# Performance work log

Hardware: AMD Instinct MI355X
Metric: run time of the kernel (lower is better)

## Reference

```python
import jax, jax.numpy as jnp
import numpy as np

D_MODEL, N, L_MAX, BATCH = 512, 64, 2048, 8


def _make_s4_buffers(n):
    # HiPPO-NPLR: hippo[i,j] = sqrt(2i+1)sqrt(2j+1) if i>j; i+1 if i==j (1-indexed)
    i = np.arange(1, n + 1)
    row = np.sqrt(2 * i + 1.0)
    hippo = np.tril(np.outer(row, row), -1) + np.diag(i + 1.0)
    p = 0.5 * np.sqrt(2 * i + 1.0)
    q = 2.0 * p
    S = -hippo + np.outer(p, q)
    lam, V = np.linalg.eig(S)
    Vc = V.conj().T
    return Vc @ p, Vc @ q, lam  # complex128 -> cast to complex64 later


def setup_inputs() -> dict:
    key = jax.random.key(0)
    k1, k2, k3, k4 = jax.random.split(key, 4)
    xavier_std = float(np.sqrt(2.0 / (N + D_MODEL)))
    p, q, lam = _make_s4_buffers(N)
    u = jax.random.normal(k1, (BATCH, L_MAX, D_MODEL), jnp.float32)
    B = jax.random.normal(k2, (D_MODEL, N), jnp.float32) * xavier_std
    Ct = jax.random.normal(k3, (D_MODEL, N), jnp.float32) * xavier_std
    D = jnp.ones((D_MODEL,), jnp.float32)
    log_step = (jax.random.uniform(k4, (D_MODEL,), jnp.float32)
                * (np.log(0.1) - np.log(0.001)) + np.log(0.001))
    return {
        "u": u, "B": B, "Ct": Ct, "D": D, "log_step": log_step,
        "p": jnp.asarray(p, jnp.complex64),
        "q": jnp.asarray(q, jnp.complex64),
        "lam": jnp.asarray(lam, jnp.complex64),
    }


def _s4_forward(u, B, Ct, D, log_step, p, q, lam):
    L = u.shape[1]  # l_max
    omega = jnp.exp((2j * np.pi / L) * jnp.arange(L)).astype(jnp.complex64)  # (L,)
    step = jnp.exp(log_step)                                                 # (d,)
    g = (2.0 / step)[:, None] * ((1.0 - omega) / (1.0 + omega))[None, :]     # (d, L)
    c = 2.0 / (1.0 + omega)                                                  # (L,)
    Bc = B.astype(jnp.complex64)
    Ctc = Ct.astype(jnp.complex64)  # Ct is real -> conj is identity
    v00 = Ctc * Bc                              # (d, n)
    v01 = Ctc * p[None, :]                      # (d, n)
    v10 = jnp.conj(q)[None, :] * Bc             # (d, n)
    v11 = jnp.broadcast_to(jnp.conj(q) * p, v00.shape)
    V = jnp.stack([v00, v01, v10, v11], 0)      # (4, d, n)
    # fused Cauchy reduction: k[k,d,l] = sum_n V[k,d,n] / (g[d,l] - lam[n])
    recip = 1.0 / (g[:, :, None] - lam[None, None, :])  # (d, L, n) big intermediate
    k00, k01, k10, k11 = jnp.einsum('kdn,dln->kdl', V, recip)
    at_roots = c * (k00 - k01 * k10 / (1.0 + k11))      # (d, L)
    # ifft + index reversal (i -> (L - i) mod L), keep real part
    order = (L - jnp.arange(L)) % L
    K = jnp.fft.ifft(at_roots, n=L, axis=-1)[:, order].real.astype(jnp.float32)  # (d, L)
    # non-circular convolution via length-2L FFT
    ud = jnp.fft.rfft(jnp.pad(u, ((0, 0), (0, L), (0, 0))), axis=1)   # (B, L+1, d)
    Kd = jnp.fft.rfft(jnp.pad(K, ((0, 0), (0, L))), axis=-1)          # (d, L+1)
    y = jnp.fft.irfft(jnp.swapaxes(ud, 1, 2) * Kd[None], axis=-1)[..., :L]  # (B, d, L)
    return jnp.swapaxes(y, 1, 2) + D[None, None, :] * u


def reference(u, B, Ct, D, log_step, p, q, lam):
    return _s4_forward(u, B, Ct, D, log_step, p, q, lam)
```

## Files before the change

### kernel.cpp

```cpp
#include <hip/hip_runtime.h>
#include <math.h>

#define D_MODEL 512
#define NSTATE  64
#define LSEQ    2048
#define L2X     4096
#define NBATCH  8
#define NT      512

#define SQ2H 0.70710678118654752f
#define C16  0.92387953251128674f
#define S16  0.38268343236508977f
#define A4096 (-1.5339807878856412e-3f)

__device__ __forceinline__ float2 cmulf(float2 a, float2 b) {
    return make_float2(a.x * b.x - a.y * b.y, a.x * b.y + a.y * b.x);
}
__device__ __forceinline__ float2 cmulc(float2 a, float2 w) {
    return make_float2(a.x * w.x + a.y * w.y, a.y * w.x - a.x * w.y);
}
__device__ __forceinline__ float2 cadd(float2 a, float2 b) { return make_float2(a.x + b.x, a.y + b.y); }
__device__ __forceinline__ float2 csub(float2 a, float2 b) { return make_float2(a.x - b.x, a.y - b.y); }
__device__ __forceinline__ float rcpf(float x) { return __builtin_amdgcn_rcpf(x); }
__device__ __forceinline__ float2 cdiv_fast(float2 a, float2 b) {
    float inv = rcpf(b.x * b.x + b.y * b.y);
    return make_float2((a.x * b.x + a.y * b.y) * inv, (a.y * b.x - a.x * b.y) * inv);
}
__device__ __forceinline__ int finitef(float v) {
    return (v == v) && (v < 3.0e38f) && (v > -3.0e38f);
}
__device__ __forceinline__ int hexrev12(int x) {
    return ((x & 15) << 8) | (x & 240) | ((x >> 8) & 15);
}

__device__ __forceinline__ int tidx(int i) { return i + (i >> 4); }
__device__ __forceinline__ int kswz(int i) { return i ^ (i >> 6); }

#define TW_SZ  1088
#define BUF_SZ 4352

__device__ __forceinline__ float2 twget4(const float2* tw, int k) {
    float2 w = tw[tidx(k & 1023)];
    if (k & 1024) w = make_float2(w.y, -w.x);
    if (k & 2048) w = make_float2(-w.x, -w.y);
    return w;
}
__device__ __forceinline__ void build_tw(float2* tw) {
    for (int k = threadIdx.x; k < 1024; k += NT) {
        float s, c;
        sincosf(A4096 * (float)k, &s, &c);
        tw[tidx(k)] = make_float2(c, s);
    }
}

__device__ __forceinline__ float2 ldc(const float* f, int n, int mode) {
    if (mode == 0) return make_float2(f[n], 0.0f);
    if (mode == 1) return make_float2(f[n], f[64 + n]);
    return make_float2(f[2 * n], f[2 * n + 1]);
}

__device__ __forceinline__ void dft4f(float2 a, float2 b, float2 c, float2 d, float2* F) {
    float2 t0 = cadd(a, c), t1 = csub(a, c);
    float2 t2 = cadd(b, d), t3 = csub(b, d);
    F[0] = cadd(t0, t2);
    F[1] = make_float2(t1.x + t3.y, t1.y - t3.x);
    F[2] = csub(t0, t2);
    F[3] = make_float2(t1.x - t3.y, t1.y + t3.x);
}
__device__ __forceinline__ void dft4i(float2 a, float2 b, float2 c, float2 d, float2* F) {
    float2 t0 = cadd(a, c), t1 = csub(a, c);
    float2 t2 = cadd(b, d), t3 = csub(b, d);
    F[0] = cadd(t0, t2);
    F[1] = make_float2(t1.x - t3.y, t1.y + t3.x);
    F[2] = csub(t0, t2);
    F[3] = make_float2(t1.x + t3.y, t1.y - t3.x);
}
__device__ __forceinline__ void dft8f(const float2* a, float2* X) {
    float2 E[4], O[4];
    dft4f(a[0], a[2], a[4], a[6], E);
    dft4f(a[1], a[3], a[5], a[7], O);
    float2 o1 = make_float2(SQ2H * (O[1].x + O[1].y), SQ2H * (O[1].y - O[1].x));
    float2 o2 = make_float2(O[2].y, -O[2].x);
    float2 o3 = make_float2(SQ2H * (O[3].y - O[3].x), -SQ2H * (O[3].x + O[3].y));
    X[0] = cadd(E[0], O[0]); X[4] = csub(E[0], O[0]);
    X[1] = cadd(E[1], o1);   X[5] = csub(E[1], o1);
    X[2] = cadd(E[2], o2);   X[6] = csub(E[2], o2);
    X[3] = cadd(E[3], o3);   X[7] = csub(E[3], o3);
}
__device__ __forceinline__ void dft8i(const float2* a, float2* X) {
    float2 E[4], O[4];
    dft4i(a[0], a[2], a[4], a[6], E);
    dft4i(a[1], a[3], a[5], a[7], O);
    float2 o1 = make_float2(SQ2H * (O[1].x - O[1].y), SQ2H * (O[1].y + O[1].x));
    float2 o2 = make_float2(-O[2].y, O[2].x);
    float2 o3 = make_float2(-SQ2H * (O[3].x + O[3].y), SQ2H * (O[3].x - O[3].y));
    X[0] = cadd(E[0], O[0]); X[4] = csub(E[0], O[0]);
    X[1] = cadd(E[1], o1);   X[5] = csub(E[1], o1);
    X[2] = cadd(E[2], o2);   X[6] = csub(E[2], o2);
    X[3] = cadd(E[3], o3);   X[7] = csub(E[3], o3);
}
__device__ __forceinline__ void dft16f(const float2* a, float2* X) {
    float2 ev[8], od[8], E[8], O[8];
    #pragma unroll
    for (int r = 0; r < 8; r++) { ev[r] = a[2 * r]; od[r] = a[2 * r + 1]; }
    dft8f(ev, E); dft8f(od, O);
    float2 t0 = O[0];
    float2 t1 = cmulf(O[1], make_float2(C16, -S16));
    float2 t2 = make_float2(SQ2H * (O[2].x + O[2].y), SQ2H * (O[2].y - O[2].x));
    float2 t3 = cmulf(O[3], make_float2(S16, -C16));
    float2 t4 = make_float2(O[4].y, -O[4].x);
    float2 t5 = cmulf(O[5], make_float2(-S16, -C16));
    float2 t6 = make_float2(SQ2H * (O[6].y - O[6].x), -SQ2H * (O[6].x + O[6].y));
    float2 t7 = cmulf(O[7], make_float2(-C16, -S16));
    X[0] = cadd(E[0], t0); X[8]  = csub(E[0], t0);
    X[1] = cadd(E[1], t1); X[9]  = csub(E[1], t1);
    X[2] = cadd(E[2], t2); X[10] = csub(E[2], t2);
    X[3] = cadd(E[3], t3); X[11] = csub(E[3], t3);
    X[4] = cadd(E[4], t4); X[12] = csub(E[4], t4);
    X[5] = cadd(E[5], t5); X[13] = csub(E[5], t5);
    X[6] = cadd(E[6], t6); X[14] = csub(E[6], t6);
    X[7] = cadd(E[7], t7); X[15] = csub(E[7], t7);
}
__device__ __forceinline__ void dft16i(const float2* a, float2* X) {
    float2 ev[8], od[8], E[8], O[8];
    #pragma unroll
    for (int r = 0; r < 8; r++) { ev[r] = a[2 * r]; od[r] = a[2 * r + 1]; }
    dft8i(ev, E); dft8i(od, O);
    float2 t0 = O[0];
    float2 t1 = cmulf(O[1], make_float2(C16, S16));
    float2 t2 = make_float2(SQ2H * (O[2].x - O[2].y), SQ2H * (O[2].x + O[2].y));
    float2 t3 = cmulf(O[3], make_float2(S16, C16));
    float2 t4 = make_float2(-O[4].y, O[4].x);
    float2 t5 = cmulf(O[5], make_float2(-S16, C16));
    float2 t6 = make_float2(-SQ2H * (O[6].x + O[6].y), SQ2H * (O[6].x - O[6].y));
    float2 t7 = cmulf(O[7], make_float2(-C16, S16));
    X[0] = cadd(E[0], t0); X[8]  = csub(E[0], t0);
    X[1] = cadd(E[1], t1); X[9]  = csub(E[1], t1);
    X[2] = cadd(E[2], t2); X[10] = csub(E[2], t2);
    X[3] = cadd(E[3], t3); X[11] = csub(E[3], t3);
    X[4] = cadd(E[4], t4); X[12] = csub(E[4], t4);
    X[5] = cadd(E[5], t5); X[13] = csub(E[5], t5);
    X[6] = cadd(E[6], t6); X[14] = csub(E[6], t6);
    X[7] = cadd(E[7], t7); X[15] = csub(E[7], t7);
}

template<int H, bool TW>
__device__ __forceinline__ void r16_dif_ld(float2* buf, const float2* twp, int t) {
    const int j = t & (H - 1);
    const int i0 = ((t - j) << 4) + j;
    const int base = i0 + (i0 >> 4);
    constexpr int S = (H >= 16) ? (H + (H >> 4)) : 1;
    float2 a[16], X[16];
    #pragma unroll
    for (int k = 0; k < 16; k++) a[k] = buf[base + k * S];
    dft16f(a, X);
    buf[base] = X[0];
    #pragma unroll
    for (int m = 1; m < 16; m++) {
        float2 v = X[m];
        if (TW) v = cmulf(v, twp[(m - 1) * 16 + j]);
        buf[base + m * S] = v;
    }
}
template<int H, bool TW>
__device__ __forceinline__ void r16_dit_ld(float2* buf, const float2* twp, int t) {
    const int j = t & (H - 1);
    const int i0 = ((t - j) << 4) + j;
    const int base = i0 + (i0 >> 4);
    constexpr int S = (H >= 16) ? (H + (H >> 4)) : 1;
    float2 a[16], X[16];
    a[0] = buf[base];
    #pragma unroll
    for (int k = 1; k < 16; k++) {
        float2 v = buf[base + k * S];
        if (TW) v = cmulc(v, twp[(k - 1) * 16 + j]);
        a[k] = v;
    }
    dft16i(a, X);
    #pragma unroll
    for (int m = 0; m < 16; m++) buf[base + m * S] = X[m];
}

template<int H, int F, int TWMODE, int NBF>
__device__ __forceinline__ void r8_dif_stage(float2* buf, const float2* tw, const float2* twp) {
    __syncthreads();
    const int tid = threadIdx.x;
    if (NBF >= NT || tid < NBF) {
        const int j = tid & (H - 1);
        const int i0 = ((tid - j) << 3) + j;
        float2 a[8], X[8];
        #pragma unroll
        for (int k = 0; k < 8; k++) a[k] = buf[tidx(i0 + k * H)];
        dft8f(a, X);
        if (TWMODE == 1) {
            #pragma unroll
            for (int m = 1; m < 8; m++) X[m] = cmulf(X[m], twp[(m - 1) * H + j]);
        } else if (TWMODE == 2) {
            #pragma unroll
            for (int m = 1; m < 8; m++) X[m] = cmulf(X[m], twget4(tw, (j * F * m) & 4095));
        }
        #pragma unroll
        for (int m = 0; m < 8; m++) buf[tidx(i0 + m * H)] = X[m];
    }
}
__device__ __forceinline__ void r4_dif_h1(float2* buf) {
    __syncthreads();
    const int tid = threadIdx.x;
    const int i0 = tid << 2;
    float2 F[4];
    dft4f(buf[tidx(i0)], buf[tidx(i0 + 1)], buf[tidx(i0 + 2)], buf[tidx(i0 + 3)], F);
    #pragma unroll
    for (int m = 0; m < 4; m++) buf[tidx(i0 + m)] = F[m];
}

__global__ __launch_bounds__(NT) void s4_khat_kernel(
    const float* __restrict__ Bmat, const float* __restrict__ Ct,
    const float* __restrict__ log_step,
    const float* __restrict__ pf, const float* __restrict__ qf,
    const float* __restrict__ lf,
    float2* __restrict__ Khat, int size_hint)
{
    __shared__ float2 tw[TW_SZ];
    __shared__ float2 buf[BUF_SZ];
    __shared__ float2 stash[289];
    __shared__ float2 twK2[224];
    __shared__ float2 twK3[28];
    __shared__ float2 twp2[240];
    const int d = blockIdx.x;
    const int tid = threadIdx.x;

    build_tw(tw);
    if (tid < 224) { int m = (tid >> 5) + 1, j = tid & 31; float s, c;
        sincosf(A4096 * (float)(16 * j * m), &s, &c); twK2[tid] = make_float2(c, s); }
    else if (tid < 252) { int r = tid - 224; int m = (r >> 3) + 1, j = r & 7; float s, c;
        sincosf(A4096 * (float)(128 * j * m), &s, &c); twK3[r] = make_float2(c, s); }
    else if (tid < 492) { int r = tid - 252; int m = (r >> 4) + 1, j = r & 15; float s, c;
        sincosf(A4096 * (float)(16 * j * m), &s, &c); twp2[r] = make_float2(c, s); }

    int mode;
    if (size_hint >= 128) {
        mode = (fabsf(lf[1] + 0.5f) < 0.05f) ? 1 : 2;
    } else {
        float s1 = 0.0f, s2 = 0.0f;
        bool ok = true;
        for (int n = 0; n < 64; n++) {
            float v = lf[64 + n];
            if (!finitef(v)) { ok = false; break; }
            s1 += v; s2 += fabsf(v);
        }
        mode = (ok && s2 > 0.5f && s2 < 1.0e6f && fabsf(s1) < 1.0e-2f * s2) ? 1 : 0;
    }

    float2* v01  = stash;
    float2* v10  = stash + 64;
    float2* v11  = stash + 128;
    float2* lamS = stash + 192;
    float*  v00  = (float*)(stash + 256);

    if (tid < NSTATE) {
        int n = tid;
        float Bdn = Bmat[d * NSTATE + n];
        float Cdn = Ct[d * NSTATE + n];
        float2 pn = ldc(pf, n, mode);
        float2 qn = ldc(qf, n, mode);
        float2 qc = make_float2(qn.x, -qn.y);
        v00[n]  = Cdn * Bdn;
        v01[n]  = make_float2(Cdn * pn.x, Cdn * pn.y);
        v10[n]  = make_float2(qc.x * Bdn, qc.y * Bdn);
        v11[n]  = cmulf(qc, pn);
        lamS[n] = ldc(lf, n, mode);
    }
    const float two_over_step = 2.0f / expf(log_step[d]);
    __syncthreads();

    float gyr[2], tanl[2];
    float2 a00[2], a01[2], a10[2], a11[2];
    #pragma unroll
    for (int i = 0; i < 2; i++) {
        int l = tid + i * NT;
        float2 w = twget4(tw, 2 * l);
        float cth = w.x, sth = -w.y;
        float tl = sth * rcpf(1.0f + cth);
        tanl[i] = tl;
        gyr[i]  = -two_over_step * tl;
        a00[i] = make_float2(0.f, 0.f); a01[i] = make_float2(0.f, 0.f);
        a10[i] = make_float2(0.f, 0.f); a11[i] = make_float2(0.f, 0.f);
    }
    for (int n = 0; n < NSTATE; n++) {
        float2 ln = lamS[n];
        float  c0 = v00[n];
        float2 c1 = v01[n], c2 = v10[n], c3 = v11[n];
        float dxn = -ln.x;
        float dx2 = ln.x * ln.x;
        #pragma unroll
        for (int i = 0; i < 2; i++) {
            float dy = gyr[i] - ln.y;
            float ir = rcpf(fmaf(dy, dy, dx2));
            float rx = dxn * ir, ry = -dy * ir;
            a00[i].x += c0 * rx;               a00[i].y += c0 * ry;
            a01[i].x += c1.x * rx - c1.y * ry; a01[i].y += c1.x * ry + c1.y * rx;
            a10[i].x += c2.x * rx - c2.y * ry; a10[i].y += c2.x * ry + c2.y * rx;
            a11[i].x += c3.x * rx - c3.y * ry; a11[i].y += c3.x * ry + c3.y * rx;
        }
    }
    __syncthreads();
    #pragma unroll
    for (int i = 0; i < 2; i++) {
        int l = tid + i * NT;
        float2 cl = make_float2(1.0f, -tanl[i]);
        float2 onep = make_float2(1.0f + a11[i].x, a11[i].y);
        float2 corr = cdiv_fast(cmulf(a01[i], a10[i]), onep);
        float2 ar = cmulf(cl, csub(a00[i], corr));
        if (!finitef(ar.x) || !finitef(ar.y)) ar = make_float2(0.0f, 0.0f);
        buf[tidx(l)] = ar;
        if (l > 0) buf[tidx(2048 - l)] = make_float2(ar.x, -ar.y);
    }
    if (tid == 0) buf[tidx(1024)] = make_float2(0.0f, 0.0f);

    r8_dif_stage<256, 2, 2, 256>(buf, tw, nullptr);
    r8_dif_stage<32, 0, 1, 256>(buf, tw, twK2);
    r8_dif_stage<4, 0, 1, 256>(buf, tw, twK3);
    r4_dif_h1(buf);
    __syncthreads();

    const float inv2048 = 1.0f / 2048.0f;
    float krv[4]; int tpos[4];
    #pragma unroll
    for (int i = 0; i < 4; i++) {
        int p = tid + i * NT;
        tpos[i] = (p >> 8) | (((p >> 5) & 7) << 3) | (((p >> 2) & 7) << 6) | ((p & 3) << 9);
        krv[i] = buf[tidx(p)].x * inv2048;
    }
    __syncthreads();
    float* kfp = (float*)buf;
    #pragma unroll
    for (int i = 0; i < 4; i++) kfp[kswz(tpos[i])] = krv[i];
    __syncthreads();

    float a8[8];
    if (tid < 256) {
        #pragma unroll
        for (int k = 0; k < 8; k++) a8[k] = kfp[kswz(tid + 256 * k)];
    }
    __syncthreads();
    if (tid < 256) {
        const int j = tid;
        float2 ar8[8], bq[8], E[8], O[8], X[16];
        #pragma unroll
        for (int k = 0; k < 8; k++) ar8[k] = make_float2(a8[k], 0.0f);
        dft8f(ar8, E);
        bq[0] = make_float2(a8[0], 0.0f);
        bq[1] = make_float2(C16 * a8[1], -S16 * a8[1]);
        bq[2] = make_float2(SQ2H * a8[2], -SQ2H * a8[2]);
        bq[3] = make_float2(S16 * a8[3], -C16 * a8[3]);
        bq[4] = make_float2(0.0f, -a8[4]);
        bq[5] = make_float2(-S16 * a8[5], -C16 * a8[5]);
        bq[6] = make_float2(-SQ2H * a8[6], -SQ2H * a8[6]);
        bq[7] = make_float2(-C16 * a8[7], -S16 * a8[7]);
        dft8f(bq, O);
        #pragma unroll
        for (int r = 0; r < 8; r++) { X[2 * r] = E[r]; X[2 * r + 1] = O[r]; }
        const int base = j + (j >> 4);
        buf[base] = X[0];
        #pragma unroll
        for (int m = 1; m < 16; m++)
            buf[base + 272 * m] = cmulf(X[m], twget4(tw, j * m));
    }
    __syncthreads();
    if (tid < 256) r16_dif_ld<16, true>(buf, twp2, tid);
    __syncthreads();
    if (tid < 256) r16_dif_ld<1, false>(buf, nullptr, tid);
    __syncthreads();

    const float inv4096 = 1.0f / 4096.0f;
    for (int k = tid; k < L2X; k += NT) {
        float2 v = buf[tidx(k)];
        float vx = v.x * inv4096, vy = v.y * inv4096;
        if (!finitef(vx)) vx = 0.0f;
        if (!finitef(vy)) vy = 0.0f;
        Khat[(size_t)d * L2X + k] = make_float2(vx, vy);
    }
}

__global__ __launch_bounds__(NT) void conv_kernel(
    const float* __restrict__ u, const float2* __restrict__ Khat,
    const float* __restrict__ Dvec, float* __restrict__ out)
{
    __shared__ float2 tw[TW_SZ];
    __shared__ float2 bufs[2 * BUF_SZ];
    __shared__ float2 twp2[240];
    const int blk = blockIdx.x;
    const int d0 = blk >> 2;
    const int bp = blk & 3;
    const int tid = threadIdx.x;
    const int half = tid >> 8;
    const int jj = tid & 255;
    const int b = bp * 2 + half;
    float2* buf = bufs + half * BUF_SZ;

    build_tw(tw);
    if (tid < 240) { int m = (tid >> 4) + 1, j = tid & 15; float s, c;
        sincosf(A4096 * (float)(16 * j * m), &s, &c); twp2[tid] = make_float2(c, s); }

    const float* ub = u + (size_t)b * LSEQ * D_MODEL + 2 * d0;
    float2 ureg[8];
    #pragma unroll
    for (int k = 0; k < 8; k++)
        ureg[k] = *(const float2*)(ub + (size_t)(jj + 256 * k) * D_MODEL);

    __syncthreads();

    {
        float2 E[8], O[8], bq[8], X[16];
        dft8f(ureg, E);
        bq[0] = ureg[0];
        bq[1] = cmulf(ureg[1], make_float2(C16, -S16));
        bq[2] = make_float2(SQ2H * (ureg[2].x + ureg[2].y), SQ2H * (ureg[2].y - ureg[2].x));
        bq[3] = cmulf(ureg[3], make_float2(S16, -C16));
        bq[4] = make_float2(ureg[4].y, -ureg[4].x);
        bq[5] = cmulf(ureg[5], make_float2(-S16, -C16));
        bq[6] = make_float2(SQ2H * (ureg[6].y - ureg[6].x), -SQ2H * (ureg[6].x + ureg[6].y));
        bq[7] = cmulf(ureg[7], make_float2(-C16, -S16));
        dft8f(bq, O);
        #pragma unroll
        for (int r = 0; r < 8; r++) { X[2 * r] = E[r]; X[2 * r + 1] = O[r]; }
        const int base = jj + (jj >> 4);
        buf[base] = X[0];
        #pragma unroll
        for (int m = 1; m < 16; m++)
            buf[base + 272 * m] = cmulf(X[m], twget4(tw, jj * m));
    }
    __syncthreads();
    r16_dif_ld<16, true>(buf, twp2, jj);
    __syncthreads();
    r16_dif_ld<1, false>(buf, nullptr, jj);
    __syncthreads();

    const float2* K0 = Khat + (size_t)(2 * d0) * L2X;
    const float2* K1 = K0 + L2X;
    for (int t0 = jj; t0 < L2X; t0 += 256) {
        int fr = hexrev12(t0);
        int jm = hexrev12((L2X - fr) & (L2X - 1));
        if (t0 > jm) continue;
        float2 Zk = buf[tidx(t0)], Zm = buf[tidx(jm)];
        float2 U0 = make_float2(0.5f * (Zk.x + Zm.x), 0.5f * (Zk.y - Zm.y));
        float2 U1 = make_float2(0.5f * (Zk.y + Zm.y), 0.5f * (Zm.x - Zk.x));
        float2 Y0 = cmulf(U0, K0[t0]);
        float2 Y1 = cmulf(U1, K1[t0]);
        buf[tidx(t0)] = make_float2(Y0.x - Y1.y, Y0.y + Y1.x);
        buf[tidx(jm)] = make_float2(Y0.x + Y1.y, Y1.x - Y0.y);
    }
    __syncthreads();
    r16_dit_ld<1, false>(buf, nullptr, jj);
    __syncthreads();
    r16_dit_ld<16, true>(buf, twp2, jj);
    __syncthreads();

    const float dv0 = Dvec[2 * d0];
    const float dv1 = Dvec[2 * d0 + 1];
    {
        const int base = jj + (jj >> 4);
        float2 a[16];
        a[0] = buf[base];
        #pragma unroll
        for (int k = 1; k < 16; k++)
            a[k] = cmulc(buf[base + 272 * k], twget4(tw, jj * k));
        float2 ev[8], od[8], E[8], O[8];
        #pragma unroll
        for (int r = 0; r < 8; r++) { ev[r] = a[2 * r]; od[r] = a[2 * r + 1]; }
        dft8i(ev, E); dft8i(od, O);
        float2 t[8];
        t[0] = O[0];
        t[1] = cmulf(O[1], make_float2(C16, S16));
        t[2] = make_float2(SQ2H * (O[2].x - O[2].y), SQ2H * (O[2].x + O[2].y));
        t[3] = cmulf(O[3], make_float2(S16, C16));
        t[4] = make_float2(-O[4].y, O[4].x);
        t[5] = cmulf(O[5], make_float2(-S16, C16));
        t[6] = make_float2(-SQ2H * (O[6].x + O[6].y), SQ2H * (O[6].x - O[6].y));
        t[7] = cmulf(O[7], make_float2(-C16, S16));
        #pragma unroll
        for (int m = 0; m < 8; m++) {
            float2 y = cadd(E[m], t[m]);
            float o0 = y.x + dv0 * ureg[m].x;
            float o1 = y.y + dv1 * ureg[m].y;
            if (!finitef(o0)) o0 = 4.0e5f;
            if (!finitef(o1)) o1 = 4.0e5f;
            *(float2*)(out + ((size_t)b * LSEQ + jj + 256 * m) * D_MODEL + 2 * d0) = make_float2(o0, o1);
        }
    }
}

extern "C" void kernel_launch(void* const* d_in, const int* in_sizes, int n_in,
                              void* d_out, int out_size, void* d_ws, size_t ws_size,
                              hipStream_t stream) {
    (void)n_in; (void)out_size; (void)ws_size;
    const float* u        = (const float*)d_in[0];
    const float* Bmat     = (const float*)d_in[1];
    const float* Ct       = (const float*)d_in[2];
    const float* Dvec     = (const float*)d_in[3];
    const float* log_step = (const float*)d_in[4];
    const float* pf       = (const float*)d_in[5];
    const float* qf       = (const float*)d_in[6];
    const float* lf       = (const float*)d_in[7];
    float* out = (float*)d_out;

    int size_hint = in_sizes[5];

    float2* Khat = (float2*)d_ws;

    s4_khat_kernel<<<D_MODEL, NT, 0, stream>>>(Bmat, Ct, log_step, pf, qf, lf, Khat, size_hint);
    conv_kernel<<<NBATCH * (D_MODEL / 4), NT, 0, stream>>>(u, Khat, Dvec, out);
}
```

Baseline: 184.5 us.

## Shrink conv blocks to one batch and replace twiddle table with recurrence

The convolution kernel now runs 256-thread blocks that each handle one batch element and one channel pair, instead of 512-thread blocks covering two batches. The shared-memory twiddle table built per block is dropped, and the outer-stage twiddles are computed by repeated complex multiplication of a per-thread base twiddle from one sincosf. This cuts shared memory and table setup per block and allows more resident blocks. In exchange the recurrence adds a serial chain of complex multiplies, slight precision drift, and more blocks each reading Khat.

```diff
diff --git a/kernel.cpp b/kernel.cpp
--- a/kernel.cpp
+++ b/kernel.cpp
@@ -7,6 +7,7 @@
 #define L2X     4096
 #define NBATCH  8
 #define NT      512
+#define CNT     256
 
 #define SQ2H 0.70710678118654752f
 #define C16  0.92387953251128674f
@@ -382,25 +383,23 @@
     }
 }
 
-__global__ __launch_bounds__(NT) void conv_kernel(
+__global__ __launch_bounds__(CNT) void conv_kernel(
     const float* __restrict__ u, const float2* __restrict__ Khat,
     const float* __restrict__ Dvec, float* __restrict__ out)
 {
-    __shared__ float2 tw[TW_SZ];
-    __shared__ float2 bufs[2 * BUF_SZ];
+    __shared__ float2 buf[BUF_SZ];
     __shared__ float2 twp2[240];
     const int blk = blockIdx.x;
-    const int d0 = blk >> 2;
-    const int bp = blk & 3;
-    const int tid = threadIdx.x;
-    const int half = tid >> 8;
-    const int jj = tid & 255;
-    const int b = bp * 2 + half;
-    float2* buf = bufs + half * BUF_SZ;
-
-    build_tw(tw);
-    if (tid < 240) { int m = (tid >> 4) + 1, j = tid & 15; float s, c;
-        sincosf(A4096 * (float)(16 * j * m), &s, &c); twp2[tid] = make_float2(c, s); }
+    const int d0 = blk >> 3;
+    const int b  = blk & 7;
+    const int jj = threadIdx.x;
+
+    if (jj < 240) { int m = (jj >> 4) + 1, j = jj & 15; float s, c;
+        sincosf(A4096 * (float)(16 * j * m), &s, &c); twp2[jj] = make_float2(c, s); }
+
+    float sj, cj;
+    sincosf(A4096 * (float)jj, &sj, &cj);
+    const float2 w1 = make_float2(cj, sj);
 
     const float* ub = u + (size_t)b * LSEQ * D_MODEL + 2 * d0;
     float2 ureg[8];
@@ -426,9 +425,12 @@
         for (int r = 0; r < 8; r++) { X[2 * r] = E[r]; X[2 * r + 1] = O[r]; }
         const int base = jj + (jj >> 4);
         buf[base] = X[0];
-        #pragma unroll
-        for (int m = 1; m < 16; m++)
-            buf[base + 272 * m] = cmulf(X[m], twget4(tw, jj * m));
+        float2 wm = w1;
+        #pragma unroll
+        for (int m = 1; m < 16; m++) {
+            buf[base + 272 * m] = cmulf(X[m], wm);
+            wm = cmulf(wm, w1);
+        }
     }
     __syncthreads();
     r16_dif_ld<16, true>(buf, twp2, jj);
@@ -438,7 +440,7 @@
 
     const float2* K0 = Khat + (size_t)(2 * d0) * L2X;
     const float2* K1 = K0 + L2X;
-    for (int t0 = jj; t0 < L2X; t0 += 256) {
+    for (int t0 = jj; t0 < L2X; t0 += CNT) {
         int fr = hexrev12(t0);
         int jm = hexrev12((L2X - fr) & (L2X - 1));
         if (t0 > jm) continue;
@@ -462,9 +464,12 @@
         const int base = jj + (jj >> 4);
         float2 a[16];
         a[0] = buf[base];
-        #pragma unroll
-        for (int k = 1; k < 16; k++)
-            a[k] = cmulc(buf[base + 272 * k], twget4(tw, jj * k));
+        float2 wk = w1;
+        #pragma unroll
+        for (int k = 1; k < 16; k++) {
+            a[k] = cmulc(buf[base + 272 * k], wk);
+            wk = cmulf(wk, w1);
+        }
         float2 ev[8], od[8], E[8], O[8];
         #pragma unroll
         for (int r = 0; r < 8; r++) { ev[r] = a[2 * r]; od[r] = a[2 * r + 1]; }
@@ -509,5 +514,5 @@
     float2* Khat = (float2*)d_ws;
 
     s4_khat_kernel<<<D_MODEL, NT, 0, stream>>>(Bmat, Ct, log_step, pf, qf, lf, Khat, size_hint);
-    conv_kernel<<<NBATCH * (D_MODEL / 4), NT, 0, stream>>>(u, Khat, Dvec, out);
-}
+    conv_kernel<<<NBATCH * (D_MODEL / 2), CNT, 0, stream>>>(u, Khat, Dvec, out);
+}
```

Result: faster. 179.9 us (-2.5%).
